# Kernel tuning notes

Measured on AMD Instinct MI355X. Metric: run time of the kernel, lower is better.

The kernel has to match this reference:

```python
import jax, jax.numpy as jnp
import numpy as np

NT, NB, NC = 64, 1024, 512
H, E, NCLS = 512, 128, 97


def gru_cell(x, h, w_ih, w_hh, b_ih, b_hh):
    # torch.nn.GRUCell semantics; gate order r, z, n
    gi = x @ w_ih.T + b_ih
    gh = h @ w_hh.T + b_hh
    ir, iz, inn = jnp.split(gi, 3, axis=1)
    hr, hz, hn = jnp.split(gh, 3, axis=1)
    r = jax.nn.sigmoid(ir + hr)
    z = jax.nn.sigmoid(iz + hz)
    n = jnp.tanh(inn + r * hn)
    return (1.0 - z) * n + z * h


def setup_inputs() -> dict:
    key = jax.random.key(0)
    ks = jax.random.split(key, 12)
    s = 0.02
    return {
        'feats': jax.random.normal(ks[0], (NT, NB, NC), jnp.float32),
        'w_i2h': jax.random.normal(ks[1], (H, NC), jnp.float32) * s,
        'w_h2h': jax.random.normal(ks[2], (H, H), jnp.float32) * s,
        'b_h2h': jnp.zeros((H,), jnp.float32),
        'w_score': jax.random.normal(ks[3], (1, H), jnp.float32) * s,
        'w_ih': jax.random.normal(ks[4], (3 * H, NC + E), jnp.float32) * s,
        'w_hh': jax.random.normal(ks[5], (3 * H, H), jnp.float32) * s,
        'b_ih': jnp.zeros((3 * H,), jnp.float32),
        'b_hh': jnp.zeros((3 * H,), jnp.float32),
        'char_emb': jax.random.normal(ks[6], (NCLS + 1, E), jnp.float32),
        'w_gen': jax.random.normal(ks[7], (NCLS, H), jnp.float32) * s,
        'b_gen': jnp.zeros((NCLS,), jnp.float32),
        'text_length': jax.random.randint(ks[8], (NB,), 1, 33),
    }


def reference(feats, w_i2h, w_h2h, b_h2h, w_score, w_ih, w_hh, b_ih, b_hh,
              char_emb, w_gen, b_gen, text_length):
    # Attention.forward with test=True (greedy decode)
    nT, nB, nC = feats.shape
    tl = np.asarray(text_length)
    num_steps = int(tl.max())

    # i2h(feats) is identical every step -> hoist out of the loop
    feats_proj = jnp.einsum('tbc,hc->tbh', feats, w_i2h)  # [T,B,H]

    def step(carry, _):
        hidden, tgt = carry  # hidden [B,H], tgt [B] int
        hproj = hidden @ w_h2h.T + b_h2h                     # [B,H]
        e = jnp.tanh(feats_proj + hproj[None]) @ w_score[0]  # [T,B]
        alpha = jax.nn.softmax(e, axis=0)                    # softmax over nT
        context = jnp.einsum('tbc,tb->bc', feats, alpha)     # [B,C]
        x = jnp.concatenate([context, char_emb[tgt]], axis=1)  # [B,C+E]
        new_hidden = gru_cell(x, hidden, w_ih, w_hh, b_ih, b_hh)
        logits = new_hidden @ w_gen.T + b_gen                # [B,NCLS]
        new_tgt = jnp.argmax(logits, axis=1) + 1
        return (new_hidden, new_tgt), logits

    h0 = jnp.zeros((nB, w_h2h.shape[0]), feats.dtype)
    t0 = jnp.zeros((nB,), jnp.int32)
    _, probs = jax.lax.scan(step, (h0, t0), None, length=num_steps)  # [S,B,NCLS]
    probs = probs.transpose(1, 0, 2)  # [B,S,NCLS]

    # ragged gather: first text_length[b] steps of each batch element
    b_idx = np.repeat(np.arange(nB), tl)
    t_idx = np.concatenate([np.arange(l) for l in tl])
    return probs[b_idx, t_idx]  # [num_labels, NCLS]
```

## Files before the change

kernel.cpp:

```cpp
#include <hip/hip_runtime.h>
#include <math.h>

#define NT 64
#define NB 1024
#define NC 512
#define HH 512
#define EE 128
#define NCLS 97
#define STEPS 32

#define LDSW 80

typedef __bf16 bf16_t;
typedef bf16_t bf16x8 __attribute__((ext_vector_type(8)));
typedef float f32x4 __attribute__((ext_vector_type(4)));
typedef unsigned short u16x8 __attribute__((ext_vector_type(8)));

__device__ __forceinline__ float fast_tanh(float x) {
  float e = __expf(2.f * x);
  return 1.f - 2.f / (e + 1.f);
}
__device__ __forceinline__ float fast_sig(float x) {
  return 1.f / (1.f + __expf(-x));
}

__device__ __forceinline__ unsigned short bf16_rne(float x) {
  unsigned u = __float_as_uint(x);
  unsigned r = u + 0x7FFFu + ((u >> 16) & 1u);
  return (unsigned short)(r >> 16);
}
__device__ __forceinline__ void split2(float x, unsigned short& h,
                                       unsigned short& l) {
  unsigned u = __float_as_uint(x);
  h = (unsigned short)(u >> 16);
  float hf = __uint_as_float(u & 0xFFFF0000u);
  l = bf16_rne(x - hf);
}

__global__ __launch_bounds__(256) void gemm_mfma_big(
    const float* __restrict__ A, const unsigned short* __restrict__ Bhg,
    const unsigned short* __restrict__ Blg, float* __restrict__ C, int N,
    int K) {
  __shared__ __attribute__((aligned(16))) char Ah[128 * LDSW];
  __shared__ __attribute__((aligned(16))) char Al[128 * LDSW];
  __shared__ __attribute__((aligned(16))) char Bh[128 * LDSW];
  __shared__ __attribute__((aligned(16))) char Bl[128 * LDSW];
  const int bm = blockIdx.y * 128;
  const int bn = blockIdx.x * 128;
  const int tid = threadIdx.x;
  const int sr = tid >> 1;
  const int sq = (tid & 1) * 16;
  const int lane = tid & 63, wid = tid >> 6;
  const int wm = (wid >> 1) * 64, wn = (wid & 1) * 64;
  const int lr = lane & 15;
  const int ks = (lane >> 4) * 16;

  const float* Ap = A + (size_t)(bm + sr) * K + sq;
  const unsigned short* Bph = Bhg + (size_t)(bn + sr) * K + sq;
  const unsigned short* Bpl = Blg + (size_t)(bn + sr) * K + sq;

  f32x4 acc[4][4];
  f32x4 z;
  z[0] = 0.f; z[1] = 0.f; z[2] = 0.f; z[3] = 0.f;
#pragma unroll
  for (int i = 0; i < 4; ++i)
#pragma unroll
    for (int j = 0; j < 4; ++j) acc[i][j] = z;

  float4 pa[4];
  u16x8 pbh[2], pbl[2];
#pragma unroll
  for (int f = 0; f < 4; ++f) pa[f] = *(const float4*)(Ap + f * 4);
#pragma unroll
  for (int g = 0; g < 2; ++g) {
    pbh[g] = *(const u16x8*)(Bph + g * 8);
    pbl[g] = *(const u16x8*)(Bpl + g * 8);
  }

  for (int k0 = 0; k0 < K; k0 += 32) {
#pragma unroll
    for (int f = 0; f < 4; ++f) {
      ushort4 h4, l4;
      split2(pa[f].x, h4.x, l4.x);
      split2(pa[f].y, h4.y, l4.y);
      split2(pa[f].z, h4.z, l4.z);
      split2(pa[f].w, h4.w, l4.w);
      int off = sr * LDSW + sq * 2 + f * 8;
      *(ushort4*)(Ah + off) = h4;
      *(ushort4*)(Al + off) = l4;
    }
#pragma unroll
    for (int g = 0; g < 2; ++g) {
      int off = sr * LDSW + sq * 2 + g * 16;
      *(u16x8*)(Bh + off) = pbh[g];
      *(u16x8*)(Bl + off) = pbl[g];
    }
    __syncthreads();
    if (k0 + 32 < K) {
#pragma unroll
      for (int f = 0; f < 4; ++f)
        pa[f] = *(const float4*)(Ap + k0 + 32 + f * 4);
#pragma unroll
      for (int g = 0; g < 2; ++g) {
        pbh[g] = *(const u16x8*)(Bph + k0 + 32 + g * 8);
        pbl[g] = *(const u16x8*)(Bpl + k0 + 32 + g * 8);
      }
    }
    bf16x8 a_h[4], a_l[4], b_h[4], b_l[4];
#pragma unroll
    for (int mf = 0; mf < 4; ++mf) {
      int ro = (wm + mf * 16 + lr) * LDSW + ks;
      a_h[mf] = *(const bf16x8*)(Ah + ro);
      a_l[mf] = *(const bf16x8*)(Al + ro);
    }
#pragma unroll
    for (int nf = 0; nf < 4; ++nf) {
      int ro = (wn + nf * 16 + lr) * LDSW + ks;
      b_h[nf] = *(const bf16x8*)(Bh + ro);
      b_l[nf] = *(const bf16x8*)(Bl + ro);
    }
#pragma unroll
    for (int mf = 0; mf < 4; ++mf)
#pragma unroll
      for (int nf = 0; nf < 4; ++nf)
        acc[mf][nf] = __builtin_amdgcn_mfma_f32_16x16x32_bf16(
            a_h[mf], b_h[nf], acc[mf][nf], 0, 0, 0);
#pragma unroll
    for (int mf = 0; mf < 4; ++mf)
#pragma unroll
      for (int nf = 0; nf < 4; ++nf)
        acc[mf][nf] = __builtin_amdgcn_mfma_f32_16x16x32_bf16(
            a_h[mf], b_l[nf], acc[mf][nf], 0, 0, 0);
#pragma unroll
    for (int mf = 0; mf < 4; ++mf)
#pragma unroll
      for (int nf = 0; nf < 4; ++nf)
        acc[mf][nf] = __builtin_amdgcn_mfma_f32_16x16x32_bf16(
            a_l[mf], b_h[nf], acc[mf][nf], 0, 0, 0);
    __syncthreads();
  }
#pragma unroll
  for (int mf = 0; mf < 4; ++mf) {
    int row0 = bm + wm + mf * 16 + (lane >> 4) * 4;
#pragma unroll
    for (int nf = 0; nf < 4; ++nf) {
      int col = bn + wn + nf * 16 + lr;
      float* Cp = C + (size_t)row0 * N + col;
      Cp[0] = acc[mf][nf][0];
      Cp[N] = acc[mf][nf][1];
      Cp[2 * N] = acc[mf][nf][2];
      Cp[3 * N] = acc[mf][nf][3];
    }
  }
}

__global__ __launch_bounds__(256) void gemm_mfma_step(
    const float* __restrict__ A, int lda, const unsigned short* __restrict__ Bhg,
    const unsigned short* __restrict__ Blg, const float* __restrict__ bias,
    float* __restrict__ Ca, float* __restrict__ Cb, int ldc,
    const int* __restrict__ cnt, int step) {
  const int bm = blockIdx.y * 64;
  if (bm >= cnt[step]) return;
  __shared__ __attribute__((aligned(16))) char Ah[64 * LDSW];
  __shared__ __attribute__((aligned(16))) char Al[64 * LDSW];
  __shared__ __attribute__((aligned(16))) char Bh[128 * LDSW];
  __shared__ __attribute__((aligned(16))) char Bl[128 * LDSW];
  const int kh = blockIdx.z;
  const int kbase = kh * 256;
  float* __restrict__ C = kh ? Cb : Ca;
  const int bn = blockIdx.x * 128;
  const int tid = threadIdx.x;
  const int ar = tid >> 2, aq = (tid & 3) * 8;
  const int br = tid >> 1, bq = (tid & 1) * 16;
  const int lane = tid & 63, wid = tid >> 6;
  const int wm = (wid >> 1) * 32, wn = (wid & 1) * 64;
  const int lr = lane & 15;
  const int ks = (lane >> 4) * 16;

  const float* Ap = A + (size_t)(bm + ar) * lda + kbase + aq;
  const unsigned short* Bph = Bhg + (size_t)(bn + br) * 512 + kbase + bq;
  const unsigned short* Bpl = Blg + (size_t)(bn + br) * 512 + kbase + bq;

  f32x4 acc[2][4];
  f32x4 z;
  z[0] = 0.f; z[1] = 0.f; z[2] = 0.f; z[3] = 0.f;
#pragma unroll
  for (int i = 0; i < 2; ++i)
#pragma unroll
    for (int j = 0; j < 4; ++j) acc[i][j] = z;

  float4 pa[2];
  u16x8 pbh[2], pbl[2];
  pa[0] = *(const float4*)(Ap);
  pa[1] = *(const float4*)(Ap + 4);
#pragma unroll
  for (int g = 0; g < 2; ++g) {
    pbh[g] = *(const u16x8*)(Bph + g * 8);
    pbl[g] = *(const u16x8*)(Bpl + g * 8);
  }

  for (int k0 = 0; k0 < 256; k0 += 32) {
#pragma unroll
    for (int f = 0; f < 2; ++f) {
      ushort4 h4, l4;
      float4 v = pa[f];
      split2(v.x, h4.x, l4.x);
      split2(v.y, h4.y, l4.y);
      split2(v.z, h4.z, l4.z);
      split2(v.w, h4.w, l4.w);
      int off = ar * LDSW + aq * 2 + f * 8;
      *(ushort4*)(Ah + off) = h4;
      *(ushort4*)(Al + off) = l4;
    }
#pragma unroll
    for (int g = 0; g < 2; ++g) {
      int off = br * LDSW + bq * 2 + g * 16;
      *(u16x8*)(Bh + off) = pbh[g];
      *(u16x8*)(Bl + off) = pbl[g];
    }
    __syncthreads();
    if (k0 + 32 < 256) {
      pa[0] = *(const float4*)(Ap + k0 + 32);
      pa[1] = *(const float4*)(Ap + k0 + 36);
#pragma unroll
      for (int g = 0; g < 2; ++g) {
        pbh[g] = *(const u16x8*)(Bph + k0 + 32 + g * 8);
        pbl[g] = *(const u16x8*)(Bpl + k0 + 32 + g * 8);
      }
    }
    bf16x8 a_h[2], a_l[2], b_h[4], b_l[4];
#pragma unroll
    for (int mf = 0; mf < 2; ++mf) {
      int ro = (wm + mf * 16 + lr) * LDSW + ks;
      a_h[mf] = *(const bf16x8*)(Ah + ro);
      a_l[mf] = *(const bf16x8*)(Al + ro);
    }
#pragma unroll
    for (int nf = 0; nf < 4; ++nf) {
      int ro = (wn + nf * 16 + lr) * LDSW + ks;
      b_h[nf] = *(const bf16x8*)(Bh + ro);
      b_l[nf] = *(const bf16x8*)(Bl + ro);
    }
#pragma unroll
    for (int mf = 0; mf < 2; ++mf)
#pragma unroll
      for (int nf = 0; nf < 4; ++nf)
        acc[mf][nf] = __builtin_amdgcn_mfma_f32_16x16x32_bf16(
            a_h[mf], b_h[nf], acc[mf][nf], 0, 0, 0);
#pragma unroll
    for (int mf = 0; mf < 2; ++mf)
#pragma unroll
      for (int nf = 0; nf < 4; ++nf)
        acc[mf][nf] = __builtin_amdgcn_mfma_f32_16x16x32_bf16(
            a_h[mf], b_l[nf], acc[mf][nf], 0, 0, 0);
#pragma unroll
    for (int mf = 0; mf < 2; ++mf)
#pragma unroll
      for (int nf = 0; nf < 4; ++nf)
        acc[mf][nf] = __builtin_amdgcn_mfma_f32_16x16x32_bf16(
            a_l[mf], b_h[nf], acc[mf][nf], 0, 0, 0);
    __syncthreads();
  }
  float bc[4] = {0.f, 0.f, 0.f, 0.f};
  if (bias && kh == 0) {
#pragma unroll
    for (int nf = 0; nf < 4; ++nf) bc[nf] = bias[bn + wn + nf * 16 + lr];
  }
#pragma unroll
  for (int mf = 0; mf < 2; ++mf) {
    int row0 = bm + wm + mf * 16 + (lane >> 4) * 4;
#pragma unroll
    for (int nf = 0; nf < 4; ++nf) {
      int col = bn + wn + nf * 16 + lr;
      float* Cp = C + (size_t)row0 * ldc + col;
      Cp[0] = acc[mf][nf][0] + bc[nf];
      Cp[ldc] = acc[mf][nf][1] + bc[nf];
      Cp[2 * ldc] = acc[mf][nf][2] + bc[nf];
      Cp[3 * ldc] = acc[mf][nf][3] + bc[nf];
    }
  }
}

__global__ __launch_bounds__(512) void step_attn2(
    const float* __restrict__ fp, const float* __restrict__ C1a,
    const float* __restrict__ C1b, const float* __restrict__ w_score,
    const float* __restrict__ feats, float* __restrict__ context,
    const int* __restrict__ perm, const int* __restrict__ cnt, int step) {
  const int i0 = blockIdx.x;
  if (i0 >= cnt[step]) return;
  __shared__ float es[NT];
  __shared__ float als[NT];
  const int b = perm[i0];
  const int tid = threadIdx.x;
  const int lane = tid & 63, wid = tid >> 6;
  const float* hpa = C1a + (size_t)i0 * 2048 + lane * 8;
  const float* hpb = C1b + (size_t)i0 * 2048 + lane * 8;
  float4 ha0 = *(const float4*)hpa;
  float4 ha1 = *(const float4*)(hpa + 4);
  float4 hb0 = *(const float4*)hpb;
  float4 hb1 = *(const float4*)(hpb + 4);
  float4 h0, h1;
  h0.x = ha0.x + hb0.x; h0.y = ha0.y + hb0.y;
  h0.z = ha0.z + hb0.z; h0.w = ha0.w + hb0.w;
  h1.x = ha1.x + hb1.x; h1.y = ha1.y + hb1.y;
  h1.z = ha1.z + hb1.z; h1.w = ha1.w + hb1.w;
  float4 w0 = *(const float4*)(w_score + lane * 8);
  float4 w1 = *(const float4*)(w_score + lane * 8 + 4);
#pragma unroll
  for (int pass = 0; pass < 2; ++pass) {
    float4 f0[4], f1[4];
#pragma unroll
    for (int i = 0; i < 4; ++i) {
      int t = wid * 8 + pass * 4 + i;
      const float* fr = fp + ((size_t)t * NB + b) * HH + lane * 8;
      f0[i] = *(const float4*)fr;
      f1[i] = *(const float4*)(fr + 4);
    }
#pragma unroll
    for (int i = 0; i < 4; ++i) {
      float acc = 0.f;
      acc += fast_tanh(f0[i].x + h0.x) * w0.x;
      acc += fast_tanh(f0[i].y + h0.y) * w0.y;
      acc += fast_tanh(f0[i].z + h0.z) * w0.z;
      acc += fast_tanh(f0[i].w + h0.w) * w0.w;
      acc += fast_tanh(f1[i].x + h1.x) * w1.x;
      acc += fast_tanh(f1[i].y + h1.y) * w1.y;
      acc += fast_tanh(f1[i].z + h1.z) * w1.z;
      acc += fast_tanh(f1[i].w + h1.w) * w1.w;
#pragma unroll
      for (int off = 32; off > 0; off >>= 1) acc += __shfl_down(acc, off, 64);
      if (lane == 0) es[wid * 8 + pass * 4 + i] = acc;
    }
  }
  __syncthreads();
  if (tid < 64) {
    float v = es[tid];
    float mx = v;
#pragma unroll
    for (int off = 32; off > 0; off >>= 1) mx = fmaxf(mx, __shfl_xor(mx, off, 64));
    float p = __expf(v - mx);
    float sum = p;
#pragma unroll
    for (int off = 32; off > 0; off >>= 1) sum += __shfl_xor(sum, off, 64);
    als[tid] = p / sum;
  }
  __syncthreads();
  float a0 = 0.f, a1 = 0.f, a2 = 0.f, a3 = 0.f;
  const float* fb = feats + (size_t)b * NC + tid;
#pragma unroll 4
  for (int t = 0; t < NT; t += 4) {
    a0 += als[t + 0] * fb[(size_t)(t + 0) * NB * NC];
    a1 += als[t + 1] * fb[(size_t)(t + 1) * NB * NC];
    a2 += als[t + 2] * fb[(size_t)(t + 2) * NB * NC];
    a3 += als[t + 3] * fb[(size_t)(t + 3) * NB * NC];
  }
  context[(size_t)i0 * NC + tid] = ((a0 + a1) + (a2 + a3));
}

__global__ __launch_bounds__(128) void step_update2(
    const float* __restrict__ C1a, const float* __restrict__ C1b,
    const float* __restrict__ Ga, const float* __restrict__ Gb,
    const float* __restrict__ P, const float* __restrict__ hc,
    float* __restrict__ hn_out, const float* __restrict__ w_gen,
    const float* __restrict__ b_gen, const int* __restrict__ offs,
    float* __restrict__ out, int* __restrict__ tgt,
    const int* __restrict__ perm, const int* __restrict__ cnt, int step) {
  const int i0 = blockIdx.x;
  if (i0 >= cnt[step]) return;
  __shared__ float hs[HH];
  __shared__ float lv[128];
  __shared__ int li[128];
  const int b = perm[i0];
  const int tid = threadIdx.x;
  const int tg = tgt[b];
  const float* gia = Ga + (size_t)i0 * 1536;
  const float* gib = Gb + (size_t)i0 * 1536;
  const float* Pb = P + (size_t)tg * 1536;
  const float* gha = C1a + (size_t)i0 * 2048 + 512;
  const float* ghb = C1b + (size_t)i0 * 2048 + 512;
#pragma unroll
  for (int i = 0; i < 4; ++i) {
    int j = tid + i * 128;
    float ir = gia[j] + gib[j] + Pb[j];
    float iz = gia[512 + j] + gib[512 + j] + Pb[512 + j];
    float in = gia[1024 + j] + gib[1024 + j] + Pb[1024 + j];
    float hr = gha[j] + ghb[j];
    float hz = gha[512 + j] + ghb[512 + j];
    float hnv = gha[1024 + j] + ghb[1024 + j];
    float r = fast_sig(ir + hr);
    float z = fast_sig(iz + hz);
    float n = fast_tanh(in + r * hnv);
    float h = hc[(size_t)i0 * HH + j];
    float hv = (1.f - z) * n + z * h;
    hs[j] = hv;
    hn_out[(size_t)i0 * HH + j] = hv;
  }
  __syncthreads();
  float acc = -INFINITY;
  if (tid < NCLS) {
    const float4* wr4 = (const float4*)(w_gen + (size_t)tid * HH);
    float s = 0.f;
    for (int k = 0; k < HH / 4; ++k) {
      float4 w = wr4[k];
      s += hs[4 * k + 0] * w.x + hs[4 * k + 1] * w.y +
           hs[4 * k + 2] * w.z + hs[4 * k + 3] * w.w;
    }
    acc = s + b_gen[tid];
    out[(size_t)(offs[b] + step) * NCLS + tid] = acc;
  }
  lv[tid] = acc;
  li[tid] = tid;
  __syncthreads();
  for (int d = 64; d > 0; d >>= 1) {
    if (tid < d) {
      float v2 = lv[tid + d];
      int i2 = li[tid + d];
      if (v2 > lv[tid] || (v2 == lv[tid] && i2 < li[tid])) {
        lv[tid] = v2;
        li[tid] = i2;
      }
    }
    __syncthreads();
  }
  if (tid == 0) tgt[b] = li[0] + 1;
}

__global__ __launch_bounds__(1024) void sort_tl(const int* __restrict__ tl,
                                                int* __restrict__ perm,
                                                int* __restrict__ cnt,
                                                int* __restrict__ offs) {
  __shared__ int s[NB];
  const int t = threadIdx.x;
  s[t] = tl[t];
  __syncthreads();
  const int myv = s[t];
  int pos = 0;
  int pre = 0;
  for (int b = 0; b < NB; ++b) {
    int v = s[b];
    pos += (v > myv || (v == myv && b < t)) ? 1 : 0;
    pre += (b < t) ? v : 0;
  }
  perm[pos] = t;
  offs[t] = pre;
  if (t < STEPS) {
    int c = 0;
    for (int b = 0; b < NB; ++b) c += (s[b] > t) ? 1 : 0;
    cnt[t] = c;
  }
}

__global__ __launch_bounds__(256) void build_P(
    const float* __restrict__ char_emb, const float* __restrict__ w_ih,
    const float* __restrict__ b_ih, float* __restrict__ P) {
  __shared__ float emb[EE];
  int c = blockIdx.x;
  int tid = threadIdx.x;
  if (tid < EE) emb[tid] = char_emb[c * EE + tid];
  __syncthreads();
  for (int j = tid; j < 3 * HH; j += 256) {
    const float* wr = w_ih + (size_t)j * (NC + EE) + NC;
    float s = 0.f;
    for (int k = 0; k < EE; ++k) s += emb[k] * wr[k];
    P[(size_t)c * 1536 + j] = s + b_ih[j];
  }
}

__global__ __launch_bounds__(256) void build_wcat(
    const float* __restrict__ w_h2h, const float* __restrict__ w_hh,
    const float* __restrict__ b_h2h, const float* __restrict__ b_hh,
    float* __restrict__ Wcat, float* __restrict__ bcat) {
  int idx = blockIdx.x * 256 + threadIdx.x;
  const int n1 = 512 * 512 / 4;
  float4* dst = (float4*)Wcat;
  if (idx < n1)
    dst[idx] = ((const float4*)w_h2h)[idx];
  else
    dst[idx] = ((const float4*)w_hh)[idx - n1];
  if (idx < 2048) bcat[idx] = (idx < 512) ? b_h2h[idx] : b_hh[idx - 512];
}

__global__ __launch_bounds__(256) void split512(
    const float* __restrict__ src, int ld, unsigned short* __restrict__ hi,
    unsigned short* __restrict__ lo, int rows) {
  int idx = blockIdx.x * 256 + threadIdx.x;
  if (idx >= rows * 512) return;
  int r = idx >> 9, c = idx & 511;
  float x = src[(size_t)r * ld + c];
  unsigned short h, l;
  split2(x, h, l);
  hi[idx] = h;
  lo[idx] = l;
}

__global__ __launch_bounds__(256) void init_kernel(float* __restrict__ h0,
                                                   int* __restrict__ tgt) {
  int idx = blockIdx.x * 256 + threadIdx.x;
  if (idx < NB * HH) h0[idx] = 0.f;
  if (idx < NB) tgt[idx] = 0;
}

extern "C" void kernel_launch(void* const* d_in, const int* in_sizes, int n_in,
                              void* d_out, int out_size, void* d_ws,
                              size_t ws_size, hipStream_t stream) {
  const float* feats = (const float*)d_in[0];
  const float* w_i2h = (const float*)d_in[1];
  const float* w_h2h = (const float*)d_in[2];
  const float* b_h2h = (const float*)d_in[3];
  const float* w_score = (const float*)d_in[4];
  const float* w_ih = (const float*)d_in[5];
  const float* w_hh = (const float*)d_in[6];
  const float* b_ih = (const float*)d_in[7];
  const float* b_hh = (const float*)d_in[8];
  const float* char_emb = (const float*)d_in[9];
  const float* w_gen = (const float*)d_in[10];
  const float* b_gen = (const float*)d_in[11];
  const int* tl = (const int*)d_in[12];
  float* out = (float*)d_out;

  char* ws = (char*)d_ws;
  float* fp = (float*)ws;      ws += (size_t)NT * NB * HH * 4;
  float* C1a = (float*)ws;     ws += (size_t)NB * 2048 * 4;
  float* C1b = (float*)ws;     ws += (size_t)NB * 2048 * 4;
  float* Ga = (float*)ws;      ws += (size_t)NB * 1536 * 4;
  float* Gb = (float*)ws;      ws += (size_t)NB * 1536 * 4;
  float* context = (float*)ws; ws += (size_t)NB * NC * 4;
  float* h0 = (float*)ws;      ws += (size_t)NB * HH * 4;
  float* h1 = (float*)ws;      ws += (size_t)NB * HH * 4;
  float* Wcat = (float*)ws;    ws += (size_t)2048 * 512 * 4;
  float* bcat = (float*)ws;    ws += 2048 * 4;
  float* P = (float*)ws;       ws += (size_t)98 * 1536 * 4;
  unsigned short* Wi_h = (unsigned short*)ws; ws += (size_t)512 * 512 * 2;
  unsigned short* Wi_l = (unsigned short*)ws; ws += (size_t)512 * 512 * 2;
  unsigned short* Wc_h = (unsigned short*)ws; ws += (size_t)2048 * 512 * 2;
  unsigned short* Wc_l = (unsigned short*)ws; ws += (size_t)2048 * 512 * 2;
  unsigned short* Wg_h = (unsigned short*)ws; ws += (size_t)1536 * 512 * 2;
  unsigned short* Wg_l = (unsigned short*)ws; ws += (size_t)1536 * 512 * 2;
  int* tgt = (int*)ws;         ws += 4096;
  int* offs = (int*)ws;        ws += 4096;
  int* perm = (int*)ws;        ws += 4096;
  int* cnt = (int*)ws;         ws += 4096;

  hipLaunchKernelGGL(sort_tl, dim3(1), dim3(1024), 0, stream, tl, perm, cnt,
                     offs);
  hipLaunchKernelGGL(init_kernel, dim3((NB * HH) / 256), dim3(256), 0, stream,
                     h0, tgt);
  hipLaunchKernelGGL(build_wcat, dim3(1024), dim3(256), 0, stream, w_h2h, w_hh,
                     b_h2h, b_hh, Wcat, bcat);
  hipLaunchKernelGGL(build_P, dim3(98), dim3(256), 0, stream, char_emb, w_ih,
                     b_ih, P);
  hipLaunchKernelGGL(split512, dim3(512 * 2), dim3(256), 0, stream, w_i2h, 512,
                     Wi_h, Wi_l, 512);
  hipLaunchKernelGGL(split512, dim3(2048 * 2), dim3(256), 0, stream, Wcat, 512,
                     Wc_h, Wc_l, 2048);
  hipLaunchKernelGGL(split512, dim3(1536 * 2), dim3(256), 0, stream, w_ih, 640,
                     Wg_h, Wg_l, 1536);
  hipLaunchKernelGGL(gemm_mfma_big, dim3(HH / 128, (NT * NB) / 128), dim3(256),
                     0, stream, feats, Wi_h, Wi_l, fp, HH, NC);

  float* hbuf[2] = {h0, h1};
  for (int s = 0; s < STEPS; ++s) {
    float* hc = hbuf[s & 1];
    float* hn = hbuf[(s + 1) & 1];
    hipLaunchKernelGGL(gemm_mfma_step, dim3(2048 / 128, NB / 64, 2), dim3(256),
                       0, stream, hc, HH, Wc_h, Wc_l, bcat, C1a, C1b, 2048,
                       cnt, s);
    hipLaunchKernelGGL(step_attn2, dim3(NB), dim3(512), 0, stream, fp, C1a,
                       C1b, w_score, feats, context, perm, cnt, s);
    hipLaunchKernelGGL(gemm_mfma_step, dim3(1536 / 128, NB / 64, 2), dim3(256),
                       0, stream, context, NC, Wg_h, Wg_l,
                       (const float*)nullptr, Ga, Gb, 1536, cnt, s);
    hipLaunchKernelGGL(step_update2, dim3(NB), dim3(128), 0, stream, C1a, C1b,
                       Ga, Gb, P, hc, hn, w_gen, b_gen, offs, out, tgt, perm,
                       cnt, s);
  }
}
```

Before: 2.672 ms.

## Permute feats into sorted batch order and remap big GEMM blocks per XCD

Adds a compact_feats kernel that reorders feats by the length-sorted permutation once. The hoisted projection GEMM and the attention steps then index rows by the compacted position i0 instead of gathering through perm. This lets active rows in late steps occupy a contiguous prefix of fp and fc. The big GEMM now launches a 1D grid whose block ids are swizzled so each XCD gets a contiguous band of rows. LDS stores of split bf16 A tiles are widened to 16-byte writes. The cost is an extra 128MB copy and workspace buffer.

```diff
diff --git a/kernel.cpp b/kernel.cpp
--- a/kernel.cpp
+++ b/kernel.cpp
@@ -45,8 +45,10 @@
   __shared__ __attribute__((aligned(16))) char Al[128 * LDSW];
   __shared__ __attribute__((aligned(16))) char Bh[128 * LDSW];
   __shared__ __attribute__((aligned(16))) char Bl[128 * LDSW];
-  const int bm = blockIdx.y * 128;
-  const int bn = blockIdx.x * 128;
+  const int bid = blockIdx.x;
+  const int xcd = bid & 7, idx = bid >> 3;
+  const int bm = (xcd * 64 + (idx >> 2)) * 128;
+  const int bn = (idx & 3) * 128;
   const int tid = threadIdx.x;
   const int sr = tid >> 1;
   const int sq = (tid & 1) * 16;
@@ -78,16 +80,20 @@
   }
 
   for (int k0 = 0; k0 < K; k0 += 32) {
-#pragma unroll
-    for (int f = 0; f < 4; ++f) {
-      ushort4 h4, l4;
-      split2(pa[f].x, h4.x, l4.x);
-      split2(pa[f].y, h4.y, l4.y);
-      split2(pa[f].z, h4.z, l4.z);
-      split2(pa[f].w, h4.w, l4.w);
-      int off = sr * LDSW + sq * 2 + f * 8;
-      *(ushort4*)(Ah + off) = h4;
-      *(ushort4*)(Al + off) = l4;
+    {
+      unsigned short hh[16], ll[16];
+#pragma unroll
+      for (int f = 0; f < 4; ++f) {
+        split2(pa[f].x, hh[f * 4 + 0], ll[f * 4 + 0]);
+        split2(pa[f].y, hh[f * 4 + 1], ll[f * 4 + 1]);
+        split2(pa[f].z, hh[f * 4 + 2], ll[f * 4 + 2]);
+        split2(pa[f].w, hh[f * 4 + 3], ll[f * 4 + 3]);
+      }
+      int off = sr * LDSW + sq * 2;
+      *(u16x8*)(Ah + off) = *(const u16x8*)&hh[0];
+      *(u16x8*)(Ah + off + 16) = *(const u16x8*)&hh[8];
+      *(u16x8*)(Al + off) = *(const u16x8*)&ll[0];
+      *(u16x8*)(Al + off + 16) = *(const u16x8*)&ll[8];
     }
 #pragma unroll
     for (int g = 0; g < 2; ++g) {
@@ -200,17 +206,19 @@
   }
 
   for (int k0 = 0; k0 < 256; k0 += 32) {
-#pragma unroll
-    for (int f = 0; f < 2; ++f) {
-      ushort4 h4, l4;
-      float4 v = pa[f];
-      split2(v.x, h4.x, l4.x);
-      split2(v.y, h4.y, l4.y);
-      split2(v.z, h4.z, l4.z);
-      split2(v.w, h4.w, l4.w);
-      int off = ar * LDSW + aq * 2 + f * 8;
-      *(ushort4*)(Ah + off) = h4;
-      *(ushort4*)(Al + off) = l4;
+    {
+      unsigned short hh[8], ll[8];
+      split2(pa[0].x, hh[0], ll[0]);
+      split2(pa[0].y, hh[1], ll[1]);
+      split2(pa[0].z, hh[2], ll[2]);
+      split2(pa[0].w, hh[3], ll[3]);
+      split2(pa[1].x, hh[4], ll[4]);
+      split2(pa[1].y, hh[5], ll[5]);
+      split2(pa[1].z, hh[6], ll[6]);
+      split2(pa[1].w, hh[7], ll[7]);
+      int off = ar * LDSW + aq * 2;
+      *(u16x8*)(Ah + off) = *(const u16x8*)&hh[0];
+      *(u16x8*)(Al + off) = *(const u16x8*)&ll[0];
     }
 #pragma unroll
     for (int g = 0; g < 2; ++g) {
@@ -284,13 +292,12 @@
 __global__ __launch_bounds__(512) void step_attn2(
     const float* __restrict__ fp, const float* __restrict__ C1a,
     const float* __restrict__ C1b, const float* __restrict__ w_score,
-    const float* __restrict__ feats, float* __restrict__ context,
-    const int* __restrict__ perm, const int* __restrict__ cnt, int step) {
+    const float* __restrict__ fc, float* __restrict__ context,
+    const int* __restrict__ cnt, int step) {
   const int i0 = blockIdx.x;
   if (i0 >= cnt[step]) return;
   __shared__ float es[NT];
   __shared__ float als[NT];
-  const int b = perm[i0];
   const int tid = threadIdx.x;
   const int lane = tid & 63, wid = tid >> 6;
   const float* hpa = C1a + (size_t)i0 * 2048 + lane * 8;
@@ -312,7 +319,7 @@
 #pragma unroll
     for (int i = 0; i < 4; ++i) {
       int t = wid * 8 + pass * 4 + i;
-      const float* fr = fp + ((size_t)t * NB + b) * HH + lane * 8;
+      const float* fr = fp + ((size_t)t * NB + i0) * HH + lane * 8;
       f0[i] = *(const float4*)fr;
       f1[i] = *(const float4*)(fr + 4);
     }
@@ -346,7 +353,7 @@
   }
   __syncthreads();
   float a0 = 0.f, a1 = 0.f, a2 = 0.f, a3 = 0.f;
-  const float* fb = feats + (size_t)b * NC + tid;
+  const float* fb = fc + (size_t)i0 * NC + tid;
 #pragma unroll 4
   for (int t = 0; t < NT; t += 4) {
     a0 += als[t + 0] * fb[(size_t)(t + 0) * NB * NC];
@@ -450,6 +457,19 @@
   }
 }
 
+__global__ __launch_bounds__(256) void compact_feats(
+    const float* __restrict__ feats, const int* __restrict__ perm,
+    float* __restrict__ fc) {
+  size_t idx = (size_t)blockIdx.x * 256 + threadIdx.x;
+  int c4 = (int)(idx & 127);
+  size_t row = idx >> 7;
+  int i0 = (int)(row & 1023);
+  int t = (int)(row >> 10);
+  int b = perm[i0];
+  ((float4*)fc)[idx] =
+      ((const float4*)feats)[(((size_t)t << 10) + b) * 128 + c4];
+}
+
 __global__ __launch_bounds__(256) void build_P(
     const float* __restrict__ char_emb, const float* __restrict__ w_ih,
     const float* __restrict__ b_ih, float* __restrict__ P) {
@@ -520,6 +540,7 @@
 
   char* ws = (char*)d_ws;
   float* fp = (float*)ws;      ws += (size_t)NT * NB * HH * 4;
+  float* fc = (float*)ws;      ws += (size_t)NT * NB * NC * 4;
   float* C1a = (float*)ws;     ws += (size_t)NB * 2048 * 4;
   float* C1b = (float*)ws;     ws += (size_t)NB * 2048 * 4;
   float* Ga = (float*)ws;      ws += (size_t)NB * 1536 * 4;
@@ -555,8 +576,10 @@
                      Wc_h, Wc_l, 2048);
   hipLaunchKernelGGL(split512, dim3(1536 * 2), dim3(256), 0, stream, w_ih, 640,
                      Wg_h, Wg_l, 1536);
-  hipLaunchKernelGGL(gemm_mfma_big, dim3(HH / 128, (NT * NB) / 128), dim3(256),
-                     0, stream, feats, Wi_h, Wi_l, fp, HH, NC);
+  hipLaunchKernelGGL(compact_feats, dim3((NT * NB * NC / 4) / 256), dim3(256),
+                     0, stream, feats, perm, fc);
+  hipLaunchKernelGGL(gemm_mfma_big, dim3(2048), dim3(256), 0, stream, fc,
+                     Wi_h, Wi_l, fp, HH, NC);
 
   float* hbuf[2] = {h0, h1};
   for (int s = 0; s < STEPS; ++s) {
@@ -566,7 +589,7 @@
                        0, stream, hc, HH, Wc_h, Wc_l, bcat, C1a, C1b, 2048,
                        cnt, s);
     hipLaunchKernelGGL(step_attn2, dim3(NB), dim3(512), 0, stream, fp, C1a,
-                       C1b, w_score, feats, context, perm, cnt, s);
+                       C1b, w_score, fc, context, cnt, s);
     hipLaunchKernelGGL(gemm_mfma_step, dim3(1536 / 128, NB / 64, 2), dim3(256),
                        0, stream, context, NC, Wg_h, Wg_l,
                        (const float*)nullptr, Ga, Gb, 1536, cnt, s);
```

Measured after the change: 2.816 ms. 1.05x slower.
